# Performance work log

Measured on AMD Instinct MI355X. Metric: run time of the kernel, lower is better.

The kernel has to match this reference:

```python
import jax, jax.numpy as jnp
import numpy as np

N_NODES = 50000
N_EDGES = 800000
D_IN = 256
D_OUT = 256


def setup_inputs() -> dict:
    key = jax.random.key(0)
    k1, k2, k3, k4, k5 = jax.random.split(key, 5)
    x = jax.random.normal(k1, (N_NODES, D_IN), dtype=jnp.float32)
    edge_row = jax.random.randint(k2, (N_EDGES,), 0, N_NODES, dtype=jnp.int32)
    edge_col = jax.random.randint(k3, (N_EDGES,), 0, N_NODES, dtype=jnp.int32)
    edge_vals = jax.random.uniform(k4, (N_EDGES,), dtype=jnp.float32)
    weight = jax.random.normal(k5, (D_IN, D_OUT), dtype=jnp.float32)
    bias = jnp.zeros((D_OUT,), dtype=jnp.float32)
    return {"x": x, "edge_row": edge_row, "edge_col": edge_col,
            "edge_vals": edge_vals, "weight": weight, "bias": bias}


def reference(x, edge_row, edge_col, edge_vals, weight, bias):
    # training=False, dropout=0.0 -> dropout is a no-op.
    # Dense matmul: xw = x @ W   [N, D_out]
    xw = x @ weight
    # SpMM over COO adjacency: out[r] += vals[e] * xw[c] for edge e=(r,c)
    msgs = edge_vals[:, None] * xw[edge_col]            # [E, D_out]
    out = jax.ops.segment_sum(msgs, edge_row, num_segments=N_NODES)
    # bias + activation epilogue
    return jax.nn.relu(out + bias)
```

## Files before the change

kernel.cpp:

```cpp
#include <hip/hip_runtime.h>

#define N_NODES 50000
#define N_EDGES 800000
#define D 256

#define NPART ((N_NODES + 255) / 256)
#define HBLKS ((N_EDGES / 4 + 255) / 256)
#define XBLKS ((N_NODES * D / 4 + 255) / 256)
#define WBLKS (D * D / 256)

#define NSLICE 8
#define SLICE_ROWS (N_NODES / NSLICE)
#define E4 (N_EDGES / 4)
#define SC_WGS 256
#define SC_CHUNK ((E4 + SC_WGS - 1) / SC_WGS)

typedef __attribute__((ext_vector_type(8))) short short8;
typedef __attribute__((ext_vector_type(4))) float f32x4;

typedef const __attribute__((address_space(1))) unsigned int* as1_u32p;
typedef __attribute__((address_space(3))) unsigned int* as3_u32p;

__device__ __forceinline__ unsigned short f2bf(float f) {
    unsigned int u = __float_as_uint(f);
    u = (u + 0x7fffu + ((u >> 16) & 1u)) >> 16;
    return (unsigned short)u;
}

__global__ __launch_bounds__(256) void convhist_kernel(const int4* __restrict__ erow4,
                                                       int* __restrict__ cnt,
                                                       const float4* __restrict__ x,
                                                       ushort4* __restrict__ xh,
                                                       const float* __restrict__ W,
                                                       unsigned short* __restrict__ Wt) {
    int b = blockIdx.x;
    if (b < HBLKS) {
        int i = b * 256 + threadIdx.x;
        if (i < N_EDGES / 4) {
            int4 r = erow4[i];
            atomicAdd(&cnt[r.x], 1);
            atomicAdd(&cnt[r.y], 1);
            atomicAdd(&cnt[r.z], 1);
            atomicAdd(&cnt[r.w], 1);
        }
    } else if (b < HBLKS + XBLKS) {
        int i = (b - HBLKS) * 256 + threadIdx.x;
        float4 v = x[i];
        xh[i] = make_ushort4(f2bf(v.x), f2bf(v.y), f2bf(v.z), f2bf(v.w));
    } else {
        int idx = (b - HBLKS - XBLKS) * 256 + threadIdx.x;
        int k = idx >> 8, n = idx & 255;
        Wt[n * 256 + k] = f2bf(W[idx]);
    }
}

__global__ __launch_bounds__(256) void scan_lookback_kernel(const int* __restrict__ cnt,
                                                            unsigned int* __restrict__ bstate,
                                                            int* __restrict__ row_start,
                                                            int* __restrict__ cursor) {
    __shared__ int s[256];
    __shared__ int s_off;
    int b = blockIdx.x, t = threadIdx.x;
    int idx = b * 256 + t;
    int v = (idx < N_NODES) ? cnt[idx] : 0;
    s[t] = v;
    __syncthreads();
    for (int off = 1; off < 256; off <<= 1) {
        int u = (t >= off) ? s[t - off] : 0;
        __syncthreads();
        s[t] += u;
        __syncthreads();
    }
    int incl  = s[t];
    int total = s[255];

    if (b == 0) {
        if (t == 0) {
            __hip_atomic_store(&bstate[0], (2u << 30) | (unsigned)total,
                               __ATOMIC_RELEASE, __HIP_MEMORY_SCOPE_AGENT);
            s_off = 0;
        }
    } else {
        if (t == 0)
            __hip_atomic_store(&bstate[b], (1u << 30) | (unsigned)total,
                               __ATOMIC_RELEASE, __HIP_MEMORY_SCOPE_AGENT);
        if (t < 64) {
            int run = 0;
            int p = b - 1;
            while (true) {
                int i2 = p - t;
                unsigned st = 0;
                if (i2 >= 0) {
                    do {
                        st = __hip_atomic_load(&bstate[i2], __ATOMIC_ACQUIRE,
                                               __HIP_MEMORY_SCOPE_AGENT);
                    } while ((st >> 30) == 0u);
                }
                unsigned long long mask =
                    __ballot((i2 >= 0) && ((st >> 30) == 2u));
                if (mask) {
                    int firstLane = (int)(__ffsll((long long)mask) - 1);
                    int contrib = (t <= firstLane) ? (int)(st & 0x3fffffffu) : 0;
                    for (int o = 32; o > 0; o >>= 1) contrib += __shfl_down(contrib, o);
                    if (t == 0) run += contrib;
                    break;
                } else {
                    int contrib = (i2 >= 0) ? (int)(st & 0x3fffffffu) : 0;
                    for (int o = 32; o > 0; o >>= 1) contrib += __shfl_down(contrib, o);
                    if (t == 0) run += contrib;
                    p -= 64;
                }
            }
            if (t == 0) {
                __hip_atomic_store(&bstate[b], (2u << 30) | (unsigned)(run + total),
                                   __ATOMIC_RELEASE, __HIP_MEMORY_SCOPE_AGENT);
                s_off = run;
            }
        }
    }
    __syncthreads();
    int excl = s_off + incl - v;
    if (idx < N_NODES) {
        row_start[idx] = excl;
        cursor[idx]    = excl;
    }
    if (b == 0 && t == 0) row_start[N_NODES] = N_EDGES;
}

__global__ __launch_bounds__(256) void scatter_kernel(const int4* __restrict__ erow4,
                                                      const int4* __restrict__ ecol4,
                                                      const float4* __restrict__ evals4,
                                                      int* __restrict__ cursor,
                                                      int2* __restrict__ spay) {
    int s    = blockIdx.x & (NSLICE - 1);
    int wi   = blockIdx.x >> 3;
    int lo   = s * SLICE_ROWS;
    int hi   = lo + SLICE_ROWS;
    int base = wi * SC_CHUNK;
    int end  = base + SC_CHUNK;
    if (end > E4) end = E4;

    for (int i = base + (int)threadIdx.x; i < end; i += 256) {
        int4 r = erow4[i];
        bool m0 = (r.x >= lo) & (r.x < hi);
        bool m1 = (r.y >= lo) & (r.y < hi);
        bool m2 = (r.z >= lo) & (r.z < hi);
        bool m3 = (r.w >= lo) & (r.w < hi);
        if (m0 | m1 | m2 | m3) {
            int4   c = ecol4[i];
            float4 v = evals4[i];
            if (m0) { int p = atomicAdd(&cursor[r.x], 1); spay[p] = make_int2(c.x, __float_as_int(v.x)); }
            if (m1) { int p = atomicAdd(&cursor[r.y], 1); spay[p] = make_int2(c.y, __float_as_int(v.y)); }
            if (m2) { int p = atomicAdd(&cursor[r.z], 1); spay[p] = make_int2(c.z, __float_as_int(v.z)); }
            if (m3) { int p = atomicAdd(&cursor[r.w], 1); spay[p] = make_int2(c.w, __float_as_int(v.w)); }
        }
    }
}

__global__ __launch_bounds__(256) void aggregate_kernel(const unsigned short* __restrict__ xh,
                                                        const int* __restrict__ row_start,
                                                        const int2* __restrict__ spay,
                                                        unsigned short* __restrict__ aggh) {
    int gid  = blockIdx.x * 256 + threadIdx.x;
    int row  = gid >> 6;
    int lane = threadIdx.x & 63;
    if (row >= N_NODES) return;
    int s = row_start[row];
    int e = row_start[row + 1];
    float a0 = 0.f, a1 = 0.f, a2 = 0.f, a3 = 0.f;
    int i = s;
    for (; i + 12 <= e; i += 12) {
        int2 p[12];
        uint2 q[12];
#pragma unroll
        for (int j = 0; j < 12; ++j) p[j] = spay[i + j];
#pragma unroll
        for (int j = 0; j < 12; ++j)
            q[j] = ((const uint2*)(xh + (size_t)p[j].x * D))[lane];
#pragma unroll
        for (int j = 0; j < 12; ++j) {
            float v = __int_as_float(p[j].y);
            a0 += v * __uint_as_float(q[j].x << 16);
            a1 += v * __uint_as_float(q[j].x & 0xffff0000u);
            a2 += v * __uint_as_float(q[j].y << 16);
            a3 += v * __uint_as_float(q[j].y & 0xffff0000u);
        }
    }
    for (; i + 4 <= e; i += 4) {
        int2 p[4];
        uint2 q[4];
#pragma unroll
        for (int j = 0; j < 4; ++j) p[j] = spay[i + j];
#pragma unroll
        for (int j = 0; j < 4; ++j)
            q[j] = ((const uint2*)(xh + (size_t)p[j].x * D))[lane];
#pragma unroll
        for (int j = 0; j < 4; ++j) {
            float v = __int_as_float(p[j].y);
            a0 += v * __uint_as_float(q[j].x << 16);
            a1 += v * __uint_as_float(q[j].x & 0xffff0000u);
            a2 += v * __uint_as_float(q[j].y << 16);
            a3 += v * __uint_as_float(q[j].y & 0xffff0000u);
        }
    }
    for (; i < e; ++i) {
        int2  p = spay[i];
        float v = __int_as_float(p.y);
        uint2 q = ((const uint2*)(xh + (size_t)p.x * D))[lane];
        a0 += v * __uint_as_float(q.x << 16);
        a1 += v * __uint_as_float(q.x & 0xffff0000u);
        a2 += v * __uint_as_float(q.y << 16);
        a3 += v * __uint_as_float(q.y & 0xffff0000u);
    }
    ushort4 o = make_ushort4(f2bf(a0), f2bf(a1), f2bf(a2), f2bf(a3));
    ((ushort4*)(aggh + (size_t)row * D))[lane] = o;
}

__global__ __launch_bounds__(256) void gemm_mfma(const unsigned short* __restrict__ A,
                                                 const unsigned short* __restrict__ Wt,
                                                 const float* __restrict__ bias,
                                                 float* __restrict__ out) {
    __shared__ unsigned short As[128 * 32];
    __shared__ unsigned short Bs[128 * 32];

    int t    = threadIdx.x;
    int w    = t >> 6;
    int lane = t & 63;
    int wm   = w & 1;
    int wn   = w >> 1;
    int mblk = blockIdx.x >> 1;
    int nblk = blockIdx.x & 1;
    int m0   = mblk * 128;
    int n0   = nblk * 128;

    f32x4 acc[4][4];
#pragma unroll
    for (int i = 0; i < 4; ++i)
#pragma unroll
        for (int j = 0; j < 4; ++j) acc[i][j] = (f32x4){0.f, 0.f, 0.f, 0.f};

    int lq = lane >> 2;
    int lr = lane & 3;

    for (int k0 = 0; k0 < D; k0 += 32) {
#pragma unroll
        for (int i = 0; i < 2; ++i) {
            int r0 = i * 64 + w * 16;
            int gm = m0 + r0 + lq;
            if (gm > N_NODES - 1) gm = N_NODES - 1;
            const unsigned short* gp = A + (size_t)gm * D + k0 + lr * 8;
            __builtin_amdgcn_global_load_lds((as1_u32p)gp, (as3_u32p)(As + r0 * 32), 16, 0, 0);
        }
#pragma unroll
        for (int i = 0; i < 2; ++i) {
            int r0 = i * 64 + w * 16;
            int gn = n0 + r0 + lq;
            const unsigned short* gp = Wt + (size_t)gn * D + k0 + lr * 8;
            __builtin_amdgcn_global_load_lds((as1_u32p)gp, (as3_u32p)(Bs + r0 * 32), 16, 0, 0);
        }
        __syncthreads();

        short8 af[4], bf[4];
        int kq = (lane >> 4) * 8;
        int lm = lane & 15;
#pragma unroll
        for (int mt = 0; mt < 4; ++mt)
            af[mt] = *(const short8*)(As + (wm * 64 + mt * 16 + lm) * 32 + kq);
#pragma unroll
        for (int nt = 0; nt < 4; ++nt)
            bf[nt] = *(const short8*)(Bs + (wn * 64 + nt * 16 + lm) * 32 + kq);
#pragma unroll
        for (int mt = 0; mt < 4; ++mt)
#pragma unroll
            for (int nt = 0; nt < 4; ++nt)
                acc[mt][nt] = __builtin_amdgcn_mfma_f32_16x16x32_bf16(af[mt], bf[nt], acc[mt][nt], 0, 0, 0);
        __syncthreads();
    }

    int cl = lane & 15;
    int cr = (lane >> 4) * 4;
#pragma unroll
    for (int nt = 0; nt < 4; ++nt) {
        int n = n0 + wn * 64 + nt * 16 + cl;
        float b = bias[n];
#pragma unroll
        for (int mt = 0; mt < 4; ++mt) {
            int mbase = m0 + wm * 64 + mt * 16 + cr;
#pragma unroll
            for (int r = 0; r < 4; ++r) {
                int m = mbase + r;
                if (m < N_NODES) {
                    float v = acc[mt][nt][r] + b;
                    out[(size_t)m * D + n] = v > 0.f ? v : 0.f;
                }
            }
        }
    }
}

extern "C" void kernel_launch(void* const* d_in, const int* in_sizes, int n_in,
                              void* d_out, int out_size, void* d_ws, size_t ws_size,
                              hipStream_t stream) {
    const float* x     = (const float*)d_in[0];
    const int*   erow  = (const int*)d_in[1];
    const int*   ecol  = (const int*)d_in[2];
    const float* evals = (const float*)d_in[3];
    const float* W     = (const float*)d_in[4];
    const float* bias  = (const float*)d_in[5];
    float*       out   = (float*)d_out;

    char* ws = (char*)d_ws;
    unsigned short* xh   = (unsigned short*)ws;  ws += (size_t)N_NODES * D * 2;
    unsigned short* aggh = (unsigned short*)ws;  ws += (size_t)N_NODES * D * 2;
    unsigned short* Wt   = (unsigned short*)ws;  ws += (size_t)D * D * 2;
    int* cnt             = (int*)ws;             ws += (size_t)N_NODES * sizeof(int);
    unsigned int* bstate = (unsigned int*)ws;    ws += 256 * sizeof(unsigned int);
    int* row_start       = (int*)ws;             ws += (size_t)(N_NODES + 1) * sizeof(int);
    int* cursor          = (int*)ws;             ws += (size_t)N_NODES * sizeof(int);
    ws = (char*)(((uintptr_t)ws + 15) & ~(uintptr_t)15);
    int2* spay           = (int2*)ws;

    hipMemsetAsync(cnt, 0, (size_t)N_NODES * sizeof(int) + 256 * sizeof(unsigned int), stream);

    convhist_kernel<<<HBLKS + XBLKS + WBLKS, 256, 0, stream>>>(
        (const int4*)erow, cnt, (const float4*)x, (ushort4*)xh, W, Wt);

    scan_lookback_kernel<<<NPART, 256, 0, stream>>>(cnt, bstate, row_start, cursor);

    scatter_kernel<<<NSLICE * SC_WGS, 256, 0, stream>>>(
        (const int4*)erow, (const int4*)ecol, (const float4*)evals, cursor, spay);

    int ablocks = (N_NODES * 64 + 255) / 256;
    aggregate_kernel<<<ablocks, 256, 0, stream>>>(xh, row_start, spay, aggh);

    int gblocks = ((N_NODES + 127) / 128) * 2;
    gemm_mfma<<<gblocks, 256, 0, stream>>>(aggh, Wt, bias, out);
}
```

Before: 272.9 us.

## Fuse histogram, scan and scatter into one cooperative kernel with grid syncs

Merges the conversion/histogram, look-back scan and scatter kernels into a single cooperative launch of 2048 persistent blocks that use grid.sync between phases. This removes two kernel launch boundaries and their idle gaps. The trade-off is grid-wide barrier cost, a fixed block count that requires full co-residency (launch bounds set to 8 blocks per CU), and the scatter now running with 256 work chunks per slice as before but inside the fused grid.

Result: slower. 690.4 us (+153.0%).

```diff
diff --git a/kernel.cpp b/kernel.cpp
--- a/kernel.cpp
+++ b/kernel.cpp
@@ -1,4 +1,7 @@
 #include <hip/hip_runtime.h>
+#include <hip/hip_cooperative_groups.h>
+
+namespace cg = cooperative_groups;
 
 #define N_NODES 50000
 #define N_EDGES 800000
@@ -8,11 +11,13 @@
 #define HBLKS ((N_EDGES / 4 + 255) / 256)
 #define XBLKS ((N_NODES * D / 4 + 255) / 256)
 #define WBLKS (D * D / 256)
+#define TOTB  (HBLKS + XBLKS + WBLKS)
 
 #define NSLICE 8
 #define SLICE_ROWS (N_NODES / NSLICE)
 #define E4 (N_EDGES / 4)
-#define SC_WGS 256
+#define COOP_BLOCKS 2048
+#define SC_WGS (COOP_BLOCKS / NSLICE)
 #define SC_CHUNK ((E4 + SC_WGS - 1) / SC_WGS)
 
 typedef __attribute__((ext_vector_type(8))) short short8;
@@ -27,132 +32,141 @@
     return (unsigned short)u;
 }
 
-__global__ __launch_bounds__(256) void convhist_kernel(const int4* __restrict__ erow4,
-                                                       int* __restrict__ cnt,
-                                                       const float4* __restrict__ x,
-                                                       ushort4* __restrict__ xh,
-                                                       const float* __restrict__ W,
-                                                       unsigned short* __restrict__ Wt) {
-    int b = blockIdx.x;
-    if (b < HBLKS) {
-        int i = b * 256 + threadIdx.x;
-        if (i < N_EDGES / 4) {
+__global__ __launch_bounds__(256, 8) void prep_coop(const int4* __restrict__ erow4,
+                                                    const int4* __restrict__ ecol4,
+                                                    const float4* __restrict__ evals4,
+                                                    const float4* __restrict__ x,
+                                                    ushort4* __restrict__ xh,
+                                                    const float* __restrict__ W,
+                                                    unsigned short* __restrict__ Wt,
+                                                    int* __restrict__ cnt,
+                                                    unsigned int* __restrict__ bstate,
+                                                    int* __restrict__ row_start,
+                                                    int* __restrict__ cursor,
+                                                    int2* __restrict__ spay) {
+    cg::grid_group grid = cg::this_grid();
+
+    for (int vb = blockIdx.x; vb < TOTB; vb += COOP_BLOCKS) {
+        if (vb < HBLKS) {
+            int i = vb * 256 + threadIdx.x;
+            if (i < E4) {
+                int4 r = erow4[i];
+                atomicAdd(&cnt[r.x], 1);
+                atomicAdd(&cnt[r.y], 1);
+                atomicAdd(&cnt[r.z], 1);
+                atomicAdd(&cnt[r.w], 1);
+            }
+        } else if (vb < HBLKS + XBLKS) {
+            int i = (vb - HBLKS) * 256 + threadIdx.x;
+            float4 v = x[i];
+            xh[i] = make_ushort4(f2bf(v.x), f2bf(v.y), f2bf(v.z), f2bf(v.w));
+        } else {
+            int idx = (vb - HBLKS - XBLKS) * 256 + threadIdx.x;
+            int k = idx >> 8, n = idx & 255;
+            Wt[n * 256 + k] = f2bf(W[idx]);
+        }
+    }
+
+    grid.sync();
+
+    {
+        __shared__ int s[256];
+        __shared__ int s_off;
+        int b = blockIdx.x, t = threadIdx.x;
+        if (b < NPART) {
+            int idx = b * 256 + t;
+            int v = (idx < N_NODES) ? cnt[idx] : 0;
+            s[t] = v;
+            __syncthreads();
+            for (int off = 1; off < 256; off <<= 1) {
+                int u = (t >= off) ? s[t - off] : 0;
+                __syncthreads();
+                s[t] += u;
+                __syncthreads();
+            }
+            int incl  = s[t];
+            int total = s[255];
+
+            if (b == 0) {
+                if (t == 0) {
+                    __hip_atomic_store(&bstate[0], (2u << 30) | (unsigned)total,
+                                       __ATOMIC_RELEASE, __HIP_MEMORY_SCOPE_AGENT);
+                    s_off = 0;
+                }
+            } else {
+                if (t == 0)
+                    __hip_atomic_store(&bstate[b], (1u << 30) | (unsigned)total,
+                                       __ATOMIC_RELEASE, __HIP_MEMORY_SCOPE_AGENT);
+                if (t < 64) {
+                    int run = 0;
+                    int p = b - 1;
+                    while (true) {
+                        int i2 = p - t;
+                        unsigned st = 0;
+                        if (i2 >= 0) {
+                            do {
+                                st = __hip_atomic_load(&bstate[i2], __ATOMIC_ACQUIRE,
+                                                       __HIP_MEMORY_SCOPE_AGENT);
+                            } while ((st >> 30) == 0u);
+                        }
+                        unsigned long long mask =
+                            __ballot((i2 >= 0) && ((st >> 30) == 2u));
+                        if (mask) {
+                            int firstLane = (int)(__ffsll((long long)mask) - 1);
+                            int contrib = (t <= firstLane) ? (int)(st & 0x3fffffffu) : 0;
+                            for (int o = 32; o > 0; o >>= 1) contrib += __shfl_down(contrib, o);
+                            if (t == 0) run += contrib;
+                            break;
+                        } else {
+                            int contrib = (i2 >= 0) ? (int)(st & 0x3fffffffu) : 0;
+                            for (int o = 32; o > 0; o >>= 1) contrib += __shfl_down(contrib, o);
+                            if (t == 0) run += contrib;
+                            p -= 64;
+                        }
+                    }
+                    if (t == 0) {
+                        __hip_atomic_store(&bstate[b], (2u << 30) | (unsigned)(run + total),
+                                           __ATOMIC_RELEASE, __HIP_MEMORY_SCOPE_AGENT);
+                        s_off = run;
+                    }
+                }
+            }
+            __syncthreads();
+            int excl = s_off + incl - v;
+            int idx2 = b * 256 + t;
+            if (idx2 < N_NODES) {
+                row_start[idx2] = excl;
+                cursor[idx2]    = excl;
+            }
+            if (b == 0 && t == 0) row_start[N_NODES] = N_EDGES;
+        }
+    }
+
+    grid.sync();
+
+    {
+        int sl   = blockIdx.x & (NSLICE - 1);
+        int wi   = blockIdx.x >> 3;
+        int lo   = sl * SLICE_ROWS;
+        int hi   = lo + SLICE_ROWS;
+        int base = wi * SC_CHUNK;
+        int end  = base + SC_CHUNK;
+        if (end > E4) end = E4;
+
+        for (int i = base + (int)threadIdx.x; i < end; i += 256) {
             int4 r = erow4[i];
-            atomicAdd(&cnt[r.x], 1);
-            atomicAdd(&cnt[r.y], 1);
-            atomicAdd(&cnt[r.z], 1);
-            atomicAdd(&cnt[r.w], 1);
-        }
-    } else if (b < HBLKS + XBLKS) {
-        int i = (b - HBLKS) * 256 + threadIdx.x;
-        float4 v = x[i];
-        xh[i] = make_ushort4(f2bf(v.x), f2bf(v.y), f2bf(v.z), f2bf(v.w));
-    } else {
-        int idx = (b - HBLKS - XBLKS) * 256 + threadIdx.x;
-        int k = idx >> 8, n = idx & 255;
-        Wt[n * 256 + k] = f2bf(W[idx]);
-    }
-}
-
-__global__ __launch_bounds__(256) void scan_lookback_kernel(const int* __restrict__ cnt,
-                                                            unsigned int* __restrict__ bstate,
-                                                            int* __restrict__ row_start,
-                                                            int* __restrict__ cursor) {
-    __shared__ int s[256];
-    __shared__ int s_off;
-    int b = blockIdx.x, t = threadIdx.x;
-    int idx = b * 256 + t;
-    int v = (idx < N_NODES) ? cnt[idx] : 0;
-    s[t] = v;
-    __syncthreads();
-    for (int off = 1; off < 256; off <<= 1) {
-        int u = (t >= off) ? s[t - off] : 0;
-        __syncthreads();
-        s[t] += u;
-        __syncthreads();
-    }
-    int incl  = s[t];
-    int total = s[255];
-
-    if (b == 0) {
-        if (t == 0) {
-            __hip_atomic_store(&bstate[0], (2u << 30) | (unsigned)total,
-                               __ATOMIC_RELEASE, __HIP_MEMORY_SCOPE_AGENT);
-            s_off = 0;
-        }
-    } else {
-        if (t == 0)
-            __hip_atomic_store(&bstate[b], (1u << 30) | (unsigned)total,
-                               __ATOMIC_RELEASE, __HIP_MEMORY_SCOPE_AGENT);
-        if (t < 64) {
-            int run = 0;
-            int p = b - 1;
-            while (true) {
-                int i2 = p - t;
-                unsigned st = 0;
-                if (i2 >= 0) {
-                    do {
-                        st = __hip_atomic_load(&bstate[i2], __ATOMIC_ACQUIRE,
-                                               __HIP_MEMORY_SCOPE_AGENT);
-                    } while ((st >> 30) == 0u);
-                }
-                unsigned long long mask =
-                    __ballot((i2 >= 0) && ((st >> 30) == 2u));
-                if (mask) {
-                    int firstLane = (int)(__ffsll((long long)mask) - 1);
-                    int contrib = (t <= firstLane) ? (int)(st & 0x3fffffffu) : 0;
-                    for (int o = 32; o > 0; o >>= 1) contrib += __shfl_down(contrib, o);
-                    if (t == 0) run += contrib;
-                    break;
-                } else {
-                    int contrib = (i2 >= 0) ? (int)(st & 0x3fffffffu) : 0;
-                    for (int o = 32; o > 0; o >>= 1) contrib += __shfl_down(contrib, o);
-                    if (t == 0) run += contrib;
-                    p -= 64;
-                }
-            }
-            if (t == 0) {
-                __hip_atomic_store(&bstate[b], (2u << 30) | (unsigned)(run + total),
-                                   __ATOMIC_RELEASE, __HIP_MEMORY_SCOPE_AGENT);
-                s_off = run;
-            }
-        }
-    }
-    __syncthreads();
-    int excl = s_off + incl - v;
-    if (idx < N_NODES) {
-        row_start[idx] = excl;
-        cursor[idx]    = excl;
-    }
-    if (b == 0 && t == 0) row_start[N_NODES] = N_EDGES;
-}
-
-__global__ __launch_bounds__(256) void scatter_kernel(const int4* __restrict__ erow4,
-                                                      const int4* __restrict__ ecol4,
-                                                      const float4* __restrict__ evals4,
-                                                      int* __restrict__ cursor,
-                                                      int2* __restrict__ spay) {
-    int s    = blockIdx.x & (NSLICE - 1);
-    int wi   = blockIdx.x >> 3;
-    int lo   = s * SLICE_ROWS;
-    int hi   = lo + SLICE_ROWS;
-    int base = wi * SC_CHUNK;
-    int end  = base + SC_CHUNK;
-    if (end > E4) end = E4;
-
-    for (int i = base + (int)threadIdx.x; i < end; i += 256) {
-        int4 r = erow4[i];
-        bool m0 = (r.x >= lo) & (r.x < hi);
-        bool m1 = (r.y >= lo) & (r.y < hi);
-        bool m2 = (r.z >= lo) & (r.z < hi);
-        bool m3 = (r.w >= lo) & (r.w < hi);
-        if (m0 | m1 | m2 | m3) {
-            int4   c = ecol4[i];
-            float4 v = evals4[i];
-            if (m0) { int p = atomicAdd(&cursor[r.x], 1); spay[p] = make_int2(c.x, __float_as_int(v.x)); }
-            if (m1) { int p = atomicAdd(&cursor[r.y], 1); spay[p] = make_int2(c.y, __float_as_int(v.y)); }
-            if (m2) { int p = atomicAdd(&cursor[r.z], 1); spay[p] = make_int2(c.z, __float_as_int(v.z)); }
-            if (m3) { int p = atomicAdd(&cursor[r.w], 1); spay[p] = make_int2(c.w, __float_as_int(v.w)); }
+            bool m0 = (r.x >= lo) & (r.x < hi);
+            bool m1 = (r.y >= lo) & (r.y < hi);
+            bool m2 = (r.z >= lo) & (r.z < hi);
+            bool m3 = (r.w >= lo) & (r.w < hi);
+            if (m0 | m1 | m2 | m3) {
+                int4   c = ecol4[i];
+                float4 v = evals4[i];
+                if (m0) { int p = atomicAdd(&cursor[r.x], 1); spay[p] = make_int2(c.x, __float_as_int(v.x)); }
+                if (m1) { int p = atomicAdd(&cursor[r.y], 1); spay[p] = make_int2(c.y, __float_as_int(v.y)); }
+                if (m2) { int p = atomicAdd(&cursor[r.z], 1); spay[p] = make_int2(c.z, __float_as_int(v.z)); }
+                if (m3) { int p = atomicAdd(&cursor[r.w], 1); spay[p] = make_int2(c.w, __float_as_int(v.w)); }
+            }
         }
     }
 }
@@ -322,13 +336,16 @@
 
     hipMemsetAsync(cnt, 0, (size_t)N_NODES * sizeof(int) + 256 * sizeof(unsigned int), stream);
 
-    convhist_kernel<<<HBLKS + XBLKS + WBLKS, 256, 0, stream>>>(
-        (const int4*)erow, cnt, (const float4*)x, (ushort4*)xh, W, Wt);
-
-    scan_lookback_kernel<<<NPART, 256, 0, stream>>>(cnt, bstate, row_start, cursor);
-
-    scatter_kernel<<<NSLICE * SC_WGS, 256, 0, stream>>>(
-        (const int4*)erow, (const int4*)ecol, (const float4*)evals, cursor, spay);
+    const int4*   erow4  = (const int4*)erow;
+    const int4*   ecol4  = (const int4*)ecol;
+    const float4* evals4 = (const float4*)evals;
+    const float4* x4     = (const float4*)x;
+    ushort4*      xh4    = (ushort4*)xh;
+    void* args[] = {(void*)&erow4, (void*)&ecol4, (void*)&evals4, (void*)&x4,
+                    (void*)&xh4, (void*)&W, (void*)&Wt, (void*)&cnt, (void*)&bstate,
+                    (void*)&row_start, (void*)&cursor, (void*)&spay};
+    hipLaunchCooperativeKernel((const void*)prep_coop, dim3(COOP_BLOCKS), dim3(256),
+                               args, 0, stream);
 
     int ablocks = (N_NODES * 64 + 255) / 256;
     aggregate_kernel<<<ablocks, 256, 0, stream>>>(xh, row_start, spay, aggh);
```
